# Kernel optimization log

Hardware: AMD Instinct MI355X
Metric: run time of the kernel (lower is better)

## Reference

```python
import jax, jax.numpy as jnp
import numpy as np

N = 50000
E = 800000
F_IN = 64
HID = 64


def setup_inputs() -> dict:
    key = jax.random.key(0)
    k1, k2, k3, k4, k5, k6 = jax.random.split(key, 6)
    x = jax.random.normal(k1, (N, F_IN), dtype=jnp.float32)
    edge_index = jax.random.randint(k2, (2, E), 0, N, dtype=jnp.int64)
    # GraphSAGE mean-aggregator layers: Linear(2*in -> out) applied to [x || mean_agg(x)]
    W1 = jax.random.normal(k3, (2 * F_IN, HID), dtype=jnp.float32) / np.sqrt(2 * F_IN)
    b1 = jnp.zeros((HID,), dtype=jnp.float32)
    W2 = jax.random.normal(k4, (2 * HID, HID), dtype=jnp.float32) / np.sqrt(2 * HID)
    b2 = jnp.zeros((HID,), dtype=jnp.float32)
    return {"x": x, "edge_index": edge_index, "W1": W1, "b1": b1, "W2": W2, "b2": b2}


def _sage_conv(x, src, dst, W, b):
    # mean aggregation of neighbor (src) features at dst, then linear on [self || agg]
    msg = x[src]                                                   # [E, d] gather
    s = jax.ops.segment_sum(msg, dst, num_segments=N)              # [N, d]
    cnt = jax.ops.segment_sum(jnp.ones((src.shape[0], 1), x.dtype), dst, num_segments=N)
    agg = s / jnp.maximum(cnt, 1.0)
    return jnp.concatenate([x, agg], axis=-1) @ W + b


def reference(x, edge_index, W1, b1, W2, b2):
    src, dst = edge_index[0], edge_index[1]
    h = _sage_conv(x, src, dst, W1, b1)
    h = jax.nn.relu(h)  # dropout is identity at inference
    h = _sage_conv(h, src, dst, W2, b2)
    return h
```

## Files before the change

kernel.cpp:

```cpp
#include <hip/hip_runtime.h>

#define N_NODES 50000
#define N_EDGES 800000
#define F 64
#define CHUNK 3072
#define NWG1 ((N_EDGES + CHUNK - 1) / CHUNK)
#define NBUCK 196
#define BSTRIDE 8192
#define NWTILE (N_NODES / 16)
#define NSENT N_NODES

typedef __attribute__((ext_vector_type(8))) _Float16 half8;
typedef __attribute__((ext_vector_type(4))) float f32x4;
typedef __attribute__((ext_vector_type(8))) unsigned short ushort8v;

__global__ __launch_bounds__(256) void partition_conv(
    const int*    __restrict__ src, const int* __restrict__ dst,
    const float4* __restrict__ xin,
    half8*        __restrict__ x16,
    unsigned short* __restrict__ h116,
    const float*  __restrict__ W1, const float* __restrict__ W2,
    _Float16*     __restrict__ Wt1, _Float16* __restrict__ Wt2,
    unsigned*     __restrict__ bcur,
    unsigned*     __restrict__ ebuf) {
  int t = threadIdx.x, b = blockIdx.x;
  if (b == NWG1) {
    for (int i = t; i < 64 * 128; i += 256) {
      int n = i >> 7, k = i & 127;
      Wt1[i] = (_Float16)W1[k * 64 + n];
      Wt2[i] = (_Float16)W2[k * 64 + n];
    }
    if (t < 32) ((unsigned*)(x16 + (size_t)NSENT * 8))[t] = 0;
    if (t >= 64 && t < 96) ((unsigned*)h116)[(size_t)NSENT * 32 + (t - 64)] = 0;
    return;
  }
  __shared__ int hist[256], lscan[256], lcur[256], gbase[256];
  __shared__ unsigned stage[CHUNK];
  hist[t] = 0; __syncthreads();
  int e0 = b * CHUNK;
  int cnt = N_EDGES - e0; if (cnt > CHUNK) cnt = CHUNK;
  for (int i = t; i < cnt; i += 256) atomicAdd(&hist[dst[e0 + i] >> 8], 1);

  const int TOT = N_NODES * F / 8;
  for (int i = b * 256 + t; i < TOT; i += NWG1 * 256) {
    float4 a = xin[i * 2], c = xin[i * 2 + 1];
    half8 hh;
    hh[0] = (_Float16)a.x; hh[1] = (_Float16)a.y;
    hh[2] = (_Float16)a.z; hh[3] = (_Float16)a.w;
    hh[4] = (_Float16)c.x; hh[5] = (_Float16)c.y;
    hh[6] = (_Float16)c.z; hh[7] = (_Float16)c.w;
    x16[i] = hh;
  }
  __syncthreads();

  int v = hist[t];
  lscan[t] = v; __syncthreads();
  for (int off = 1; off < 256; off <<= 1) {
    int a = (t >= off) ? lscan[t - off] : 0;
    __syncthreads();
    lscan[t] += a;
    __syncthreads();
  }
  lscan[t] -= v;
  lcur[t] = lscan[t];
  if (v > 0) gbase[t] = (int)atomicAdd(&bcur[t], (unsigned)v);
  __syncthreads();

  for (int i = t; i < cnt; i += 256) {
    int d = dst[e0 + i], s = src[e0 + i];
    int bb = d >> 8;
    int p = atomicAdd(&lcur[bb], 1);
    stage[p] = ((unsigned)bb << 24) | ((unsigned)(d & 255) << 16) | (unsigned)s;
  }
  __syncthreads();
  for (int i = t; i < cnt; i += 256) {
    unsigned e = stage[i];
    int bb = e >> 24;
    ebuf[bb * BSTRIDE + gbase[bb] + (i - lscan[bb])] = e;
  }
}

__global__ __launch_bounds__(256) void bucket_sort(
    const unsigned* __restrict__ ebuf, const unsigned* __restrict__ bcur,
    unsigned short* __restrict__ edge_src, int* __restrict__ row_start,
    int* __restrict__ deg) {
  __shared__ int lhist[128], lscan[128], lcur[128];
  __shared__ unsigned short srt[BSTRIDE / 2];
  int B = blockIdx.x, t = threadIdx.x;
  int b = B >> 1, h = B & 1;
  int s0 = b * BSTRIDE;
  int cnt = (int)bcur[b];

  if (t < 128) lhist[t] = 0;
  __syncthreads();
  for (int i = t; i < cnt; i += 256) {
    int bin = (int)((ebuf[s0 + i] >> 16) & 255);
    if ((bin >> 7) == h) atomicAdd(&lhist[bin & 127], 1);
  }
  __syncthreads();

  int v  = (t < 128) ? lhist[t] : 0;
  int pv = (v + 15) & ~15;
  if (t < 128) lscan[t] = pv;
  __syncthreads();
  for (int off = 1; off < 128; off <<= 1) {
    int a = (t >= off && t < 128) ? lscan[t - off] : 0;
    __syncthreads();
    if (t < 128) lscan[t] += a;
    __syncthreads();
  }
  if (t < 128) { lscan[t] -= pv; lcur[t] = lscan[t]; }
  __syncthreads();

  int total_p = lscan[127] + ((lhist[127] + 15) & ~15);
  int base    = h * (BSTRIDE / 2);

  for (int i = t; i < cnt; i += 256) {
    unsigned e = ebuf[s0 + i];
    int bin = (int)((e >> 16) & 255);
    if ((bin >> 7) == h) {
      int p = atomicAdd(&lcur[bin & 127], 1);
      srt[p] = (unsigned short)(e & 0xFFFFu);
    }
  }
  __syncthreads();
  if (t < 128) {
    int p0 = lscan[t];
    for (int j = v; j < pv; ++j) srt[p0 + j] = (unsigned short)NSENT;
  }
  __syncthreads();

  for (int i = t; i < total_p; i += 256) edge_src[s0 + base + i] = srt[i];

  if (t < 128) {
    int n = b * 256 + h * 128 + t;
    if (n < N_NODES) { row_start[n] = s0 + base + lscan[t]; deg[n] = v; }
  }
}

__global__ __launch_bounds__(256, 8) void sage_aggregate(
    const half8*    __restrict__ feat16,
    const int*      __restrict__ row_start,
    const int*      __restrict__ deg,
    const unsigned short* __restrict__ edge_src,
    half8*          __restrict__ mean16) {
  int t = threadIdx.x;
  int w = t >> 6, lane = t & 63;
  int o = lane >> 3, q = lane & 7;
  int n = blockIdx.x * 32 + w * 8 + o;
  if (n >= N_NODES) return;
  int start = row_start[n];
  int d     = deg[n];
  half8 acc8 = (half8){0, 0, 0, 0, 0, 0, 0, 0};
  if (d > 0) {
    const ushort8v* idp = (const ushort8v*)(edge_src + start);
    int nb = ((d + 15) & ~15) >> 3;
    ushort8v iv = idp[0];
    for (int b = 0; b < nb; ++b) {
      half8 h0 = feat16[(size_t)iv[0] * 8 + q];
      half8 h1 = feat16[(size_t)iv[1] * 8 + q];
      half8 h2 = feat16[(size_t)iv[2] * 8 + q];
      half8 h3 = feat16[(size_t)iv[3] * 8 + q];
      half8 h4 = feat16[(size_t)iv[4] * 8 + q];
      half8 h5 = feat16[(size_t)iv[5] * 8 + q];
      half8 h6 = feat16[(size_t)iv[6] * 8 + q];
      half8 h7 = feat16[(size_t)iv[7] * 8 + q];
      ushort8v nv;
      bool more = (b + 1 < nb);
      if (more) nv = idp[b + 1];
      acc8 += h0; acc8 += h1; acc8 += h2; acc8 += h3;
      acc8 += h4; acc8 += h5; acc8 += h6; acc8 += h7;
      if (more) iv = nv;
    }
  }
  float inv = (d > 0) ? 1.0f / (float)d : 0.0f;
  half8 hm;
  #pragma unroll
  for (int k = 0; k < 8; ++k) hm[k] = (_Float16)((float)acc8[k] * inv);
  mean16[(size_t)n * 8 + q] = hm;
}

__global__ __launch_bounds__(256) void sage_linear(
    const _Float16* __restrict__ self16,
    const half8*    __restrict__ mean16,
    const _Float16* __restrict__ Wt,
    const float*    __restrict__ bias,
    float*          __restrict__ outf,
    unsigned short* __restrict__ out16,
    int do_relu) {
  int t = threadIdx.x;
  int w = t >> 6, lane = t & 63;
  int wt = blockIdx.x * 4 + w;
  if (wt >= NWTILE) return;
  int m = lane & 15, quad = lane >> 4;
  size_t arow = (size_t)(wt * 16 + m) * 64 + quad * 8;
  half8 a0 = *(const half8*)(self16 + arow);
  half8 a1 = *(const half8*)(self16 + arow + 32);
  size_t mrow = (size_t)(wt * 16 + m) * 8;
  half8 a2 = mean16[mrow + quad];
  half8 a3 = mean16[mrow + quad + 4];

  #pragma unroll
  for (int nt = 0; nt < 4; ++nt) {
    float bv = bias[nt * 16 + m];
    f32x4 acc = (f32x4){bv, bv, bv, bv};
    const _Float16* wrow = Wt + (size_t)(nt * 16 + m) * 128 + quad * 8;
    half8 b0 = *(const half8*)(wrow);
    half8 b1 = *(const half8*)(wrow + 32);
    half8 b2 = *(const half8*)(wrow + 64);
    half8 b3 = *(const half8*)(wrow + 96);
    acc = __builtin_amdgcn_mfma_f32_16x16x32_f16(a0, b0, acc, 0, 0, 0);
    acc = __builtin_amdgcn_mfma_f32_16x16x32_f16(a1, b1, acc, 0, 0, 0);
    acc = __builtin_amdgcn_mfma_f32_16x16x32_f16(a2, b2, acc, 0, 0, 0);
    acc = __builtin_amdgcn_mfma_f32_16x16x32_f16(a3, b3, acc, 0, 0, 0);
    #pragma unroll
    for (int r = 0; r < 4; ++r) {
      size_t off = (size_t)(wt * 16 + quad * 4 + r) * 64 + nt * 16 + m;
      float v = acc[r];
      if (do_relu) v = fmaxf(v, 0.0f);
      if (outf)  outf[off] = v;
      if (out16) { _Float16 hv = (_Float16)v; out16[off] = *(unsigned short*)&hv; }
    }
  }
}

extern "C" void kernel_launch(void* const* d_in, const int* in_sizes, int n_in,
                              void* d_out, int out_size, void* d_ws, size_t ws_size,
                              hipStream_t stream) {
  const float* x  = (const float*)d_in[0];
  const int*   ei = (const int*)d_in[1];
  const float* W1 = (const float*)d_in[2];
  const float* b1 = (const float*)d_in[3];
  const float* W2 = (const float*)d_in[4];
  const float* b2 = (const float*)d_in[5];
  float* out = (float*)d_out;

  const int* src = ei;
  const int* dst = ei + N_EDGES;

  int* wsi       = (int*)d_ws;
  unsigned* bcur = (unsigned*)wsi;
  int* deg       = wsi + 256;
  int* row_start = wsi + 50304;
  unsigned short* edge_src = (unsigned short*)(wsi + 100352);
  unsigned* ebuf = (unsigned*)(wsi + 903168);
  half8* x16     = (half8*)(wsi + 2508800);
  unsigned short* h116 = (unsigned short*)(wsi + 4109312);
  _Float16* Wt1  = (_Float16*)(wsi + 5709824);
  _Float16* Wt2  = (_Float16*)(wsi + 5713920);
  half8* mean16  = (half8*)(wsi + 5718016);

  hipMemsetAsync(bcur, 0, 256 * sizeof(unsigned), stream);

  dim3 blk(256);
  partition_conv<<<NWG1 + 1, blk, 0, stream>>>(
      src, dst, (const float4*)x, x16, h116, W1, W2, Wt1, Wt2, bcur, ebuf);
  bucket_sort<<<NBUCK * 2, blk, 0, stream>>>(ebuf, bcur, edge_src, row_start, deg);

  dim3 grd_agg((N_NODES + 31) / 32);
  dim3 grd_lin((NWTILE + 3) / 4);

  sage_aggregate<<<grd_agg, blk, 0, stream>>>(x16, row_start, deg, edge_src, mean16);
  sage_linear<<<grd_lin, blk, 0, stream>>>((const _Float16*)x16, mean16,
                                           Wt1, b1, nullptr, h116, 1);
  sage_aggregate<<<grd_agg, blk, 0, stream>>>((const half8*)h116, row_start, deg,
                                              edge_src, mean16);
  sage_linear<<<grd_lin, blk, 0, stream>>>((const _Float16*)h116, mean16,
                                           Wt2, b2, out, nullptr, 0);
}
```

Measured before the change: 157.2 us.

## Fuse aggregation and linear per layer, sort nodes by degree within warps

Merges the mean-aggregation and MFMA linear kernels into one kernel per layer, so the mean tile stays in LDS and is never written to or read back from global memory. It also cuts the edge padding granularity from 16 to 8, which means fewer sentinel gathers. bucket_sort now builds a per-32-node permutation that orders nodes by degree, so each wave's 8 nodes have similar degree and less work is lost to divergence. In exchange, the fused kernel adds a block barrier and LDS use, runs fewer linear tiles per block, and carries extra rank computation in bucket_sort.

After: 144.8 us, median of 2. 7.8% less time.

```diff
diff --git a/kernel.cpp b/kernel.cpp
--- a/kernel.cpp
+++ b/kernel.cpp
@@ -83,7 +83,7 @@
 __global__ __launch_bounds__(256) void bucket_sort(
     const unsigned* __restrict__ ebuf, const unsigned* __restrict__ bcur,
     unsigned short* __restrict__ edge_src, int* __restrict__ row_start,
-    int* __restrict__ deg) {
+    int* __restrict__ deg, unsigned char* __restrict__ perm) {
   __shared__ int lhist[128], lscan[128], lcur[128];
   __shared__ unsigned short srt[BSTRIDE / 2];
   int B = blockIdx.x, t = threadIdx.x;
@@ -100,7 +100,7 @@
   __syncthreads();
 
   int v  = (t < 128) ? lhist[t] : 0;
-  int pv = (v + 15) & ~15;
+  int pv = (v + 7) & ~7;
   if (t < 128) lscan[t] = pv;
   __syncthreads();
   for (int off = 1; off < 128; off <<= 1) {
@@ -112,7 +112,7 @@
   if (t < 128) { lscan[t] -= pv; lcur[t] = lscan[t]; }
   __syncthreads();
 
-  int total_p = lscan[127] + ((lhist[127] + 15) & ~15);
+  int total_p = lscan[127] + ((lhist[127] + 7) & ~7);
   int base    = h * (BSTRIDE / 2);
 
   for (int i = t; i < cnt; i += 256) {
@@ -135,73 +135,86 @@
   if (t < 128) {
     int n = b * 256 + h * 128 + t;
     if (n < N_NODES) { row_start[n] = s0 + base + lscan[t]; deg[n] = v; }
-  }
-}
-
-__global__ __launch_bounds__(256, 8) void sage_aggregate(
+    int g0 = t & ~31;
+    int rank = 0;
+    #pragma unroll 8
+    for (int j = 0; j < 32; ++j) {
+      int dj = lhist[g0 + j];
+      rank += (dj < v) || (dj == v && j < (t & 31));
+    }
+    perm[b * 256 + h * 128 + g0 + rank] = (unsigned char)(t & 31);
+  }
+}
+
+__global__ __launch_bounds__(256) void sage_layer_fused(
     const half8*    __restrict__ feat16,
+    const _Float16* __restrict__ self16,
     const int*      __restrict__ row_start,
     const int*      __restrict__ deg,
     const unsigned short* __restrict__ edge_src,
-    half8*          __restrict__ mean16) {
-  int t = threadIdx.x;
-  int w = t >> 6, lane = t & 63;
-  int o = lane >> 3, q = lane & 7;
-  int n = blockIdx.x * 32 + w * 8 + o;
-  if (n >= N_NODES) return;
-  int start = row_start[n];
-  int d     = deg[n];
-  half8 acc8 = (half8){0, 0, 0, 0, 0, 0, 0, 0};
-  if (d > 0) {
-    const ushort8v* idp = (const ushort8v*)(edge_src + start);
-    int nb = ((d + 15) & ~15) >> 3;
-    ushort8v iv = idp[0];
-    for (int b = 0; b < nb; ++b) {
-      half8 h0 = feat16[(size_t)iv[0] * 8 + q];
-      half8 h1 = feat16[(size_t)iv[1] * 8 + q];
-      half8 h2 = feat16[(size_t)iv[2] * 8 + q];
-      half8 h3 = feat16[(size_t)iv[3] * 8 + q];
-      half8 h4 = feat16[(size_t)iv[4] * 8 + q];
-      half8 h5 = feat16[(size_t)iv[5] * 8 + q];
-      half8 h6 = feat16[(size_t)iv[6] * 8 + q];
-      half8 h7 = feat16[(size_t)iv[7] * 8 + q];
-      ushort8v nv;
-      bool more = (b + 1 < nb);
-      if (more) nv = idp[b + 1];
-      acc8 += h0; acc8 += h1; acc8 += h2; acc8 += h3;
-      acc8 += h4; acc8 += h5; acc8 += h6; acc8 += h7;
-      if (more) iv = nv;
-    }
-  }
-  float inv = (d > 0) ? 1.0f / (float)d : 0.0f;
-  half8 hm;
-  #pragma unroll
-  for (int k = 0; k < 8; ++k) hm[k] = (_Float16)((float)acc8[k] * inv);
-  mean16[(size_t)n * 8 + q] = hm;
-}
-
-__global__ __launch_bounds__(256) void sage_linear(
-    const _Float16* __restrict__ self16,
-    const half8*    __restrict__ mean16,
+    const unsigned char* __restrict__ perm,
     const _Float16* __restrict__ Wt,
     const float*    __restrict__ bias,
     float*          __restrict__ outf,
     unsigned short* __restrict__ out16,
     int do_relu) {
+  __shared__ _Float16 lmean[32 * 72];
   int t = threadIdx.x;
   int w = t >> 6, lane = t & 63;
-  int wt = blockIdx.x * 4 + w;
+
+  {
+    int o = lane >> 3, q = lane & 7;
+    int ln = (int)perm[blockIdx.x * 32 + w * 8 + o];
+    int n = blockIdx.x * 32 + ln;
+    if (n < N_NODES) {
+      int start = row_start[n];
+      int d     = deg[n];
+      half8 acc8 = (half8){0, 0, 0, 0, 0, 0, 0, 0};
+      if (d > 0) {
+        const ushort8v* idp = (const ushort8v*)(edge_src + start);
+        int nb = (d + 7) >> 3;
+        ushort8v iv = idp[0];
+        for (int b = 0; b < nb; ++b) {
+          half8 h0 = feat16[(size_t)iv[0] * 8 + q];
+          half8 h1 = feat16[(size_t)iv[1] * 8 + q];
+          half8 h2 = feat16[(size_t)iv[2] * 8 + q];
+          half8 h3 = feat16[(size_t)iv[3] * 8 + q];
+          half8 h4 = feat16[(size_t)iv[4] * 8 + q];
+          half8 h5 = feat16[(size_t)iv[5] * 8 + q];
+          half8 h6 = feat16[(size_t)iv[6] * 8 + q];
+          half8 h7 = feat16[(size_t)iv[7] * 8 + q];
+          ushort8v nv;
+          bool more = (b + 1 < nb);
+          if (more) nv = idp[b + 1];
+          acc8 += h0; acc8 += h1; acc8 += h2; acc8 += h3;
+          acc8 += h4; acc8 += h5; acc8 += h6; acc8 += h7;
+          if (more) iv = nv;
+        }
+      }
+      float inv = (d > 0) ? 1.0f / (float)d : 0.0f;
+      half8 hm;
+      #pragma unroll
+      for (int k = 0; k < 8; ++k) hm[k] = (_Float16)((float)acc8[k] * inv);
+      *(half8*)&lmean[ln * 72 + q * 8] = hm;
+    }
+  }
+  __syncthreads();
+
+  int tile = w >> 1;
+  int wt = blockIdx.x * 2 + tile;
   if (wt >= NWTILE) return;
   int m = lane & 15, quad = lane >> 4;
   size_t arow = (size_t)(wt * 16 + m) * 64 + quad * 8;
   half8 a0 = *(const half8*)(self16 + arow);
   half8 a1 = *(const half8*)(self16 + arow + 32);
-  size_t mrow = (size_t)(wt * 16 + m) * 8;
-  half8 a2 = mean16[mrow + quad];
-  half8 a3 = mean16[mrow + quad + 4];
-
+  int ln = tile * 16 + m;
+  half8 a2 = *(const half8*)&lmean[ln * 72 + quad * 8];
+  half8 a3 = *(const half8*)&lmean[ln * 72 + quad * 8 + 32];
+
+  int nt0 = (w & 1) * 2;
   #pragma unroll
-  for (int nt = 0; nt < 4; ++nt) {
+  for (int i = 0; i < 2; ++i) {
+    int nt = nt0 + i;
     float bv = bias[nt * 16 + m];
     f32x4 acc = (f32x4){bv, bv, bv, bv};
     const _Float16* wrow = Wt + (size_t)(nt * 16 + m) * 128 + quad * 8;
@@ -248,23 +261,22 @@
   unsigned short* h116 = (unsigned short*)(wsi + 4109312);
   _Float16* Wt1  = (_Float16*)(wsi + 5709824);
   _Float16* Wt2  = (_Float16*)(wsi + 5713920);
-  half8* mean16  = (half8*)(wsi + 5718016);
+  unsigned char* perm = (unsigned char*)(wsi + 5718016);
 
   hipMemsetAsync(bcur, 0, 256 * sizeof(unsigned), stream);
 
   dim3 blk(256);
   partition_conv<<<NWG1 + 1, blk, 0, stream>>>(
       src, dst, (const float4*)x, x16, h116, W1, W2, Wt1, Wt2, bcur, ebuf);
-  bucket_sort<<<NBUCK * 2, blk, 0, stream>>>(ebuf, bcur, edge_src, row_start, deg);
-
-  dim3 grd_agg((N_NODES + 31) / 32);
-  dim3 grd_lin((NWTILE + 3) / 4);
-
-  sage_aggregate<<<grd_agg, blk, 0, stream>>>(x16, row_start, deg, edge_src, mean16);
-  sage_linear<<<grd_lin, blk, 0, stream>>>((const _Float16*)x16, mean16,
-                                           Wt1, b1, nullptr, h116, 1);
-  sage_aggregate<<<grd_agg, blk, 0, stream>>>((const half8*)h116, row_start, deg,
-                                              edge_src, mean16);
-  sage_linear<<<grd_lin, blk, 0, stream>>>((const _Float16*)h116, mean16,
-                                           Wt2, b2, out, nullptr, 0);
-}
+  bucket_sort<<<NBUCK * 2, blk, 0, stream>>>(ebuf, bcur, edge_src, row_start,
+                                             deg, perm);
+
+  dim3 grd_fused((N_NODES + 31) / 32);
+
+  sage_layer_fused<<<grd_fused, blk, 0, stream>>>(
+      x16, (const _Float16*)x16, row_start, deg, edge_src, perm,
+      Wt1, b1, nullptr, h116, 1);
+  sage_layer_fused<<<grd_fused, blk, 0, stream>>>(
+      (const half8*)h116, (const _Float16*)h116, row_start, deg, edge_src, perm,
+      Wt2, b2, out, nullptr, 0);
+}
```
